# Optimization experiments

Hardware: AMD Instinct MI355X
Metric: run time of the kernel (lower is better)

The kernel has to match this reference:

```python
import jax, jax.numpy as jnp
import numpy as np

TOP_K = 2
NUM_EXPERTS = 64
AUX_COEF = 0.01


def setup_inputs() -> dict:
    key = jax.random.key(0)
    kx, kw = jax.random.split(key)
    B, S, D, E = 4, 4096, 2048, NUM_EXPERTS
    x = jax.random.normal(kx, (B, S, D), dtype=jnp.float32)
    # nn.Linear default init ~ U(-1/sqrt(D), 1/sqrt(D))
    W = jax.random.uniform(kw, (E, D), dtype=jnp.float32,
                           minval=-1.0 / np.sqrt(D), maxval=1.0 / np.sqrt(D))
    return {"x": x, "W": W}


def reference(x, W):
    B, S, D = x.shape
    E = W.shape[0]
    # router projection (no bias)
    logits = jnp.einsum('bsd,ed->bse', x, W)          # [B,S,E]
    probs = jax.nn.softmax(logits, axis=-1)           # [B,S,E]
    top_k_gates, top_k_indices = jax.lax.top_k(probs, TOP_K)  # [B,S,K]
    top_k_gates = top_k_gates / (jnp.sum(top_k_gates, axis=-1, keepdims=True) + 1e-9)
    # aux loss: fraction of routed slots per expert (one-hot mean) x mean router prob
    total_slots = B * S * TOP_K
    counts = jnp.zeros((E,), dtype=jnp.float32).at[top_k_indices.reshape(-1)].add(1.0)
    avg_tokens_per_expert = counts / total_slots      # == one_hot(idx).mean(dims 0,1,2)
    avg_router_prob = jnp.mean(probs, axis=(0, 1))    # [E]
    aux_loss = AUX_COEF * E * jnp.sum(avg_tokens_per_expert * avg_router_prob)
    return top_k_indices, top_k_gates, aux_loss
```

## Files before the change

### kernel.cpp

```cpp
#include <hip/hip_runtime.h>
#include <math.h>

#define NTOK 16384
#define DDIM 2048
#define NEXP 64
#define TMB  64
#define NBLK (NTOK / TMB)
#define CHF  128
#define NCHK (DDIM / CHF)

typedef _Float16 half8v __attribute__((ext_vector_type(8)));
typedef float    f32x4  __attribute__((ext_vector_type(4)));

#define MFMA16(a, b, c) __builtin_amdgcn_mfma_f32_16x16x32_f16((a), (b), (c), 0, 0, 0)

__device__ __forceinline__ void stage16(const void* g, void* l) {
    __builtin_amdgcn_global_load_lds(
        (const __attribute__((address_space(1))) unsigned int*)g,
        (__attribute__((address_space(3))) unsigned int*)l, 16, 0, 0);
}

__device__ __forceinline__ void cvt8(float4 a, float4 b, half8v& h, half8v& l) {
    h[0]=(_Float16)a.x; l[0]=(_Float16)(a.x-(float)h[0]);
    h[1]=(_Float16)a.y; l[1]=(_Float16)(a.y-(float)h[1]);
    h[2]=(_Float16)a.z; l[2]=(_Float16)(a.z-(float)h[2]);
    h[3]=(_Float16)a.w; l[3]=(_Float16)(a.w-(float)h[3]);
    h[4]=(_Float16)b.x; l[4]=(_Float16)(b.x-(float)h[4]);
    h[5]=(_Float16)b.y; l[5]=(_Float16)(b.y-(float)h[5]);
    h[6]=(_Float16)b.z; l[6]=(_Float16)(b.z-(float)h[6]);
    h[7]=(_Float16)b.w; l[7]=(_Float16)(b.w-(float)h[7]);
}

__global__ __launch_bounds__(256, 1) void router_kernel(
    const float* __restrict__ x, const float* __restrict__ W,
    float* __restrict__ accg, float* __restrict__ out)
{
    __shared__ __align__(16) float Xs[2][8192];
    __shared__ __align__(16) float Ws[2][8192];
    __shared__ float lgt[TMB][NEXP + 1];
    __shared__ float cnt[NEXP];
    __shared__ int lastBlk;

    const int tid  = threadIdx.x;
    const int lane = tid & 63;
    const int wv   = __builtin_amdgcn_readfirstlane(tid >> 6);
    const int m0   = blockIdx.x * TMB;

    if (tid < NEXP) cnt[tid] = 0.0f;

#define MKOFF(i) ({ int p_ = (i)*32 + (lane >> 1);                           \
                    int g_ = p_ ^ ((p_ >> 4) & 7);                           \
                    (g_ & 15)*2048 + (g_ >> 6)*32 + ((g_ >> 4) & 3)*8        \
                    + (lane & 1)*4; })
    const int o0 = MKOFF(0), o1 = MKOFF(1), o2 = MKOFF(2), o3 = MKOFF(3);
    const int o4 = MKOFF(4), o5 = MKOFF(5), o6 = MKOFF(6), o7 = MKOFF(7);
#undef MKOFF

    const float* bx = x + (size_t)(m0 + wv * 16) * DDIM;
    const float* bw = W + (size_t)(wv * 16) * DDIM;

#define MKP(S) ({ int g_ = (S)*64 + ((lane >> 4) << 4) + (lane & 15);        \
                  (g_ ^ ((g_ >> 4) & 7)) * 8; })
    const int pf0 = MKP(0), pf1 = MKP(1), pf2 = MKP(2), pf3 = MKP(3);
#undef MKP

    f32x4 acc0 = {0.f,0.f,0.f,0.f}, acc1 = {0.f,0.f,0.f,0.f};
    f32x4 acc2 = {0.f,0.f,0.f,0.f}, acc3 = {0.f,0.f,0.f,0.f};

#define STAGE(cc, B)                                                         \
    {                                                                        \
        const float* bx_ = bx + (size_t)(cc) * CHF;                          \
        const float* bw_ = bw + (size_t)(cc) * CHF;                          \
        float* dx_ = &Xs[B][wv * 2048];                                      \
        float* dw_ = &Ws[B][wv * 2048];                                      \
        stage16(bx_ + o0, dx_ +    0);  stage16(bw_ + o0, dw_ +    0);       \
        stage16(bx_ + o1, dx_ +  256);  stage16(bw_ + o1, dw_ +  256);       \
        stage16(bx_ + o2, dx_ +  512);  stage16(bw_ + o2, dw_ +  512);       \
        stage16(bx_ + o3, dx_ +  768);  stage16(bw_ + o3, dw_ +  768);       \
        stage16(bx_ + o4, dx_ + 1024);  stage16(bw_ + o4, dw_ + 1024);       \
        stage16(bx_ + o5, dx_ + 1280);  stage16(bw_ + o5, dw_ + 1280);       \
        stage16(bx_ + o6, dx_ + 1536);  stage16(bw_ + o6, dw_ + 1536);       \
        stage16(bx_ + o7, dx_ + 1792);  stage16(bw_ + o7, dw_ + 1792);       \
    }

#define STEP(PB, PF)                                                         \
    {                                                                        \
        float4 v0, v1;                                                       \
        half8v bh, bl;                                                       \
        v0 = *(const float4*)&Ws[PB][wv * 2048 + (PF)];                      \
        v1 = *(const float4*)&Ws[PB][wv * 2048 + (PF) + 4];                  \
        cvt8(v0, v1, bh, bl);                                                \
        half8v a0h,a0l,a1h,a1l,a2h,a2l,a3h,a3l;                              \
        v0 = *(const float4*)&Xs[PB][       (PF)];                           \
        v1 = *(const float4*)&Xs[PB][       (PF) + 4];  cvt8(v0,v1,a0h,a0l); \
        v0 = *(const float4*)&Xs[PB][2048 + (PF)];                           \
        v1 = *(const float4*)&Xs[PB][2048 + (PF) + 4];  cvt8(v0,v1,a1h,a1l); \
        v0 = *(const float4*)&Xs[PB][4096 + (PF)];                           \
        v1 = *(const float4*)&Xs[PB][4096 + (PF) + 4];  cvt8(v0,v1,a2h,a2l); \
        v0 = *(const float4*)&Xs[PB][6144 + (PF)];                           \
        v1 = *(const float4*)&Xs[PB][6144 + (PF) + 4];  cvt8(v0,v1,a3h,a3l); \
        acc0 = MFMA16(a0l, bh, acc0);                                        \
        acc0 = MFMA16(a0h, bl, acc0);                                        \
        acc0 = MFMA16(a0h, bh, acc0);                                        \
        acc1 = MFMA16(a1l, bh, acc1);                                        \
        acc1 = MFMA16(a1h, bl, acc1);                                        \
        acc1 = MFMA16(a1h, bh, acc1);                                        \
        acc2 = MFMA16(a2l, bh, acc2);                                        \
        acc2 = MFMA16(a2h, bl, acc2);                                        \
        acc2 = MFMA16(a2h, bh, acc2);                                        \
        acc3 = MFMA16(a3l, bh, acc3);                                        \
        acc3 = MFMA16(a3h, bl, acc3);                                        \
        acc3 = MFMA16(a3h, bh, acc3);                                        \
    }

#define COMPUTE(PB)                                                          \
    STEP(PB, pf0) STEP(PB, pf1) STEP(PB, pf2) STEP(PB, pf3)

    STAGE(0, 0);

    for (int cb = 0; cb < NCHK; cb += 2) {
        __syncthreads();
        STAGE(cb + 1, 1);
        COMPUTE(0);
        __syncthreads();
        if (cb + 2 < NCHK) STAGE(cb + 2, 0);
        COMPUTE(1);
    }
#undef COMPUTE
#undef STEP
#undef STAGE

    {
        const int qr = lane >> 4;
        const int nl = lane & 15;
        #pragma unroll
        for (int rr = 0; rr < 4; ++rr) {
            const int mm = qr * 4 + rr;
            lgt[ 0 + mm][wv * 16 + nl] = acc0[rr];
            lgt[16 + mm][wv * 16 + nl] = acc1[rr];
            lgt[32 + mm][wv * 16 + nl] = acc2[rr];
            lgt[48 + mm][wv * 16 + nl] = acc3[rr];
        }
    }
    __syncthreads();

    for (int pass = 0; pass < 2; ++pass) {
        const int m = pass * 32 + (tid >> 3);
        const int j = tid & 7;
        float l[8];
        #pragma unroll
        for (int i = 0; i < 8; ++i) l[i] = lgt[m][j * 8 + i];

        float mx = l[0];
        #pragma unroll
        for (int i = 1; i < 8; ++i) mx = fmaxf(mx, l[i]);
        #pragma unroll
        for (int off = 1; off < 8; off <<= 1) mx = fmaxf(mx, __shfl_xor(mx, off, 8));

        float ev[8];
        float zs = 0.f;
        float v1 = -INFINITY, v2 = -INFINITY;
        int i1 = 0, i2 = 0;
        #pragma unroll
        for (int i = 0; i < 8; ++i) {
            ev[i] = __expf(l[i] - mx);
            zs += ev[i];
            int e = j * 8 + i;
            if (l[i] > v1)      { v2 = v1; i2 = i1; v1 = l[i]; i1 = e; }
            else if (l[i] > v2) { v2 = l[i]; i2 = e; }
        }
        #pragma unroll
        for (int off = 1; off < 8; off <<= 1) zs += __shfl_xor(zs, off, 8);

        #pragma unroll
        for (int off = 1; off < 8; off <<= 1) {
            float ov1 = __shfl_xor(v1, off, 8);
            int   oi1 = __shfl_xor(i1, off, 8);
            float ov2 = __shfl_xor(v2, off, 8);
            int   oi2 = __shfl_xor(i2, off, 8);
            bool afirst = (v1 > ov1) || (v1 == ov1 && i1 < oi1);
            if (afirst) {
                bool t = (v2 > ov1) || (v2 == ov1 && i2 < oi1);
                v2 = t ? v2 : ov1;
                i2 = t ? i2 : oi1;
            } else {
                bool t = (ov2 > v1) || (ov2 == v1 && oi2 < i1);
                v2 = t ? ov2 : v1;
                i2 = t ? oi2 : i1;
                v1 = ov1;
                i1 = oi1;
            }
        }

        const float invz = 1.0f / zs;
        if (j == 0) {
            float p1 = invz;
            float p2 = __expf(v2 - mx) * invz;
            float sden = p1 + p2 + 1e-9f;
            int tokg = m0 + m;
            out[tokg * 2 + 0] = (float)i1;
            out[tokg * 2 + 1] = (float)i2;
            out[32768 + tokg * 2 + 0] = p1 / sden;
            out[32768 + tokg * 2 + 1] = p2 / sden;
            atomicAdd(&cnt[i1], 1.0f);
            atomicAdd(&cnt[i2], 1.0f);
        }

        #pragma unroll
        for (int i = 0; i < 8; ++i) lgt[m][j * 8 + i] = ev[i] * invz;
    }
    __syncthreads();

    if (tid < NEXP) {
        atomicAdd(&accg[tid], cnt[tid]);
    } else if (tid < 128) {
        int e = tid - 64;
        float s = 0.f;
        #pragma unroll
        for (int t = 0; t < TMB; ++t) s += lgt[t][e];
        atomicAdd(&accg[64 + e], s);
    }
    __syncthreads();

    if (tid == 0) {
        __threadfence();
        unsigned int old = atomicAdd((unsigned int*)(accg + 128), 1u);
        lastBlk = (old == NBLK - 1) ? 1 : 0;
    }
    __syncthreads();
    if (lastBlk && tid < 64) {
        __threadfence();
        const volatile float* ag = accg;
        float c = ag[tid];
        float p = ag[64 + tid];
        float term = (c / (float)(NTOK * 2)) * (p / (float)NTOK);
        #pragma unroll
        for (int off = 1; off < 64; off <<= 1) term += __shfl_xor(term, off, 64);
        if (tid == 0) out[65536] = 0.01f * (float)NEXP * term;
    }
}

extern "C" void kernel_launch(void* const* d_in, const int* in_sizes, int n_in,
                              void* d_out, int out_size, void* d_ws, size_t ws_size,
                              hipStream_t stream) {
    const float* x = (const float*)d_in[0];
    const float* W = (const float*)d_in[1];
    float* out  = (float*)d_out;
    float* accg = (float*)d_ws;

    hipMemsetAsync(accg, 0, 1024, stream);
    router_kernel<<<NBLK, 256, 0, stream>>>(x, W, accg, out);
}
```

Baseline: 220.7 us.

## Split K dimension across block pairs with global partial-logit reduction

Each 64-token tile is now handled by two blocks, each covering half of the hidden dimension. The grid doubles to 512 blocks, and LDS per block halves so two blocks can share a CU. Partial logits go to a global workspace, and the second block of each pair to finish (found via an atomic ticket) sums both halves and runs the softmax/top-k epilogue. The aim is better occupancy and CU fill on a grid that was too small, at the cost of extra global traffic, fences and a serialized epilogue on one block per pair.

```diff
diff --git a/kernel.cpp b/kernel.cpp
--- a/kernel.cpp
+++ b/kernel.cpp
@@ -5,9 +5,10 @@
 #define DDIM 2048
 #define NEXP 64
 #define TMB  64
-#define NBLK (NTOK / TMB)
-#define CHF  128
-#define NCHK (DDIM / CHF)
+#define NBLK 512
+#define KH   1024
+#define CHF  64
+#define NCHK (KH / CHF)
 
 typedef _Float16 half8v __attribute__((ext_vector_type(8)));
 typedef float    f32x4  __attribute__((ext_vector_type(4)));
@@ -31,37 +32,38 @@
     h[7]=(_Float16)b.w; l[7]=(_Float16)(b.w-(float)h[7]);
 }
 
-__global__ __launch_bounds__(256, 1) void router_kernel(
+__global__ __launch_bounds__(256, 2) void router_kernel(
     const float* __restrict__ x, const float* __restrict__ W,
-    float* __restrict__ accg, float* __restrict__ out)
+    float* __restrict__ accg, unsigned int* __restrict__ gtick,
+    unsigned int* __restrict__ ptick, float* __restrict__ P,
+    float* __restrict__ out)
 {
-    __shared__ __align__(16) float Xs[2][8192];
-    __shared__ __align__(16) float Ws[2][8192];
-    __shared__ float lgt[TMB][NEXP + 1];
-    __shared__ float cnt[NEXP];
-    __shared__ int lastBlk;
+    __shared__ __align__(16) float smem[16384];
+    __shared__ int winFlag, lastFlag;
+
+    float (*Xs)[4096] = (float(*)[4096])smem;
+    float (*Ws)[4096] = (float(*)[4096])(smem + 8192);
 
     const int tid  = threadIdx.x;
     const int lane = tid & 63;
     const int wv   = __builtin_amdgcn_readfirstlane(tid >> 6);
-    const int m0   = blockIdx.x * TMB;
-
-    if (tid < NEXP) cnt[tid] = 0.0f;
+    const int pair = blockIdx.x >> 1;
+    const int kh   = blockIdx.x & 1;
+    const int m0   = pair * TMB;
 
 #define MKOFF(i) ({ int p_ = (i)*32 + (lane >> 1);                           \
                     int g_ = p_ ^ ((p_ >> 4) & 7);                           \
-                    (g_ & 15)*2048 + (g_ >> 6)*32 + ((g_ >> 4) & 3)*8        \
+                    (g_ & 15)*DDIM + ((g_ >> 6) & 1)*32 + ((g_ >> 4) & 3)*8  \
                     + (lane & 1)*4; })
     const int o0 = MKOFF(0), o1 = MKOFF(1), o2 = MKOFF(2), o3 = MKOFF(3);
-    const int o4 = MKOFF(4), o5 = MKOFF(5), o6 = MKOFF(6), o7 = MKOFF(7);
 #undef MKOFF
 
-    const float* bx = x + (size_t)(m0 + wv * 16) * DDIM;
-    const float* bw = W + (size_t)(wv * 16) * DDIM;
+    const float* bx = x + (size_t)(m0 + wv * 16) * DDIM + kh * KH;
+    const float* bw = W + (size_t)(wv * 16) * DDIM + kh * KH;
 
 #define MKP(S) ({ int g_ = (S)*64 + ((lane >> 4) << 4) + (lane & 15);        \
                   (g_ ^ ((g_ >> 4) & 7)) * 8; })
-    const int pf0 = MKP(0), pf1 = MKP(1), pf2 = MKP(2), pf3 = MKP(3);
+    const int pf0 = MKP(0), pf1 = MKP(1);
 #undef MKP
 
     f32x4 acc0 = {0.f,0.f,0.f,0.f}, acc1 = {0.f,0.f,0.f,0.f};
@@ -71,34 +73,30 @@
     {                                                                        \
         const float* bx_ = bx + (size_t)(cc) * CHF;                          \
         const float* bw_ = bw + (size_t)(cc) * CHF;                          \
-        float* dx_ = &Xs[B][wv * 2048];                                      \
-        float* dw_ = &Ws[B][wv * 2048];                                      \
-        stage16(bx_ + o0, dx_ +    0);  stage16(bw_ + o0, dw_ +    0);       \
-        stage16(bx_ + o1, dx_ +  256);  stage16(bw_ + o1, dw_ +  256);       \
-        stage16(bx_ + o2, dx_ +  512);  stage16(bw_ + o2, dw_ +  512);       \
-        stage16(bx_ + o3, dx_ +  768);  stage16(bw_ + o3, dw_ +  768);       \
-        stage16(bx_ + o4, dx_ + 1024);  stage16(bw_ + o4, dw_ + 1024);       \
-        stage16(bx_ + o5, dx_ + 1280);  stage16(bw_ + o5, dw_ + 1280);       \
-        stage16(bx_ + o6, dx_ + 1536);  stage16(bw_ + o6, dw_ + 1536);       \
-        stage16(bx_ + o7, dx_ + 1792);  stage16(bw_ + o7, dw_ + 1792);       \
+        float* dx_ = &Xs[B][wv * 1024];                                      \
+        float* dw_ = &Ws[B][wv * 1024];                                      \
+        stage16(bx_ + o0, dx_ +   0);  stage16(bw_ + o0, dw_ +   0);         \
+        stage16(bx_ + o1, dx_ + 256);  stage16(bw_ + o1, dw_ + 256);         \
+        stage16(bx_ + o2, dx_ + 512);  stage16(bw_ + o2, dw_ + 512);         \
+        stage16(bx_ + o3, dx_ + 768);  stage16(bw_ + o3, dw_ + 768);         \
     }
 
 #define STEP(PB, PF)                                                         \
     {                                                                        \
         float4 v0, v1;                                                       \
         half8v bh, bl;                                                       \
-        v0 = *(const float4*)&Ws[PB][wv * 2048 + (PF)];                      \
-        v1 = *(const float4*)&Ws[PB][wv * 2048 + (PF) + 4];                  \
+        v0 = *(const float4*)&Ws[PB][wv * 1024 + (PF)];                      \
+        v1 = *(const float4*)&Ws[PB][wv * 1024 + (PF) + 4];                  \
         cvt8(v0, v1, bh, bl);                                                \
         half8v a0h,a0l,a1h,a1l,a2h,a2l,a3h,a3l;                              \
         v0 = *(const float4*)&Xs[PB][       (PF)];                           \
         v1 = *(const float4*)&Xs[PB][       (PF) + 4];  cvt8(v0,v1,a0h,a0l); \
+        v0 = *(const float4*)&Xs[PB][1024 + (PF)];                           \
+        v1 = *(const float4*)&Xs[PB][1024 + (PF) + 4];  cvt8(v0,v1,a1h,a1l); \
         v0 = *(const float4*)&Xs[PB][2048 + (PF)];                           \
-        v1 = *(const float4*)&Xs[PB][2048 + (PF) + 4];  cvt8(v0,v1,a1h,a1l); \
-        v0 = *(const float4*)&Xs[PB][4096 + (PF)];                           \
-        v1 = *(const float4*)&Xs[PB][4096 + (PF) + 4];  cvt8(v0,v1,a2h,a2l); \
-        v0 = *(const float4*)&Xs[PB][6144 + (PF)];                           \
-        v1 = *(const float4*)&Xs[PB][6144 + (PF) + 4];  cvt8(v0,v1,a3h,a3l); \
+        v1 = *(const float4*)&Xs[PB][2048 + (PF) + 4];  cvt8(v0,v1,a2h,a2l); \
+        v0 = *(const float4*)&Xs[PB][3072 + (PF)];                           \
+        v1 = *(const float4*)&Xs[PB][3072 + (PF) + 4];  cvt8(v0,v1,a3h,a3l); \
         acc0 = MFMA16(a0l, bh, acc0);                                        \
         acc0 = MFMA16(a0h, bl, acc0);                                        \
         acc0 = MFMA16(a0h, bh, acc0);                                        \
@@ -113,36 +111,58 @@
         acc3 = MFMA16(a3h, bh, acc3);                                        \
     }
 
-#define COMPUTE(PB)                                                          \
-    STEP(PB, pf0) STEP(PB, pf1) STEP(PB, pf2) STEP(PB, pf3)
-
     STAGE(0, 0);
-
     for (int cb = 0; cb < NCHK; cb += 2) {
         __syncthreads();
         STAGE(cb + 1, 1);
-        COMPUTE(0);
+        STEP(0, pf0) STEP(0, pf1)
         __syncthreads();
         if (cb + 2 < NCHK) STAGE(cb + 2, 0);
-        COMPUTE(1);
-    }
-#undef COMPUTE
+        STEP(1, pf0) STEP(1, pf1)
+    }
 #undef STEP
 #undef STAGE
 
     {
         const int qr = lane >> 4;
         const int nl = lane & 15;
+        float* gp = P + (size_t)blockIdx.x * 4096 + (qr * 4) * NEXP + wv * 16 + nl;
         #pragma unroll
         for (int rr = 0; rr < 4; ++rr) {
-            const int mm = qr * 4 + rr;
-            lgt[ 0 + mm][wv * 16 + nl] = acc0[rr];
-            lgt[16 + mm][wv * 16 + nl] = acc1[rr];
-            lgt[32 + mm][wv * 16 + nl] = acc2[rr];
-            lgt[48 + mm][wv * 16 + nl] = acc3[rr];
-        }
-    }
-    __syncthreads();
+            gp[(     rr) * NEXP] = acc0[rr];
+            gp[(16 + rr) * NEXP] = acc1[rr];
+            gp[(32 + rr) * NEXP] = acc2[rr];
+            gp[(48 + rr) * NEXP] = acc3[rr];
+        }
+    }
+    __threadfence();
+    __syncthreads();
+    if (tid == 0) {
+        unsigned int old = atomicAdd(&ptick[pair], 1u);
+        winFlag = (old == 1u);
+    }
+    __syncthreads();
+    if (!winFlag) return;
+
+    __threadfence();
+    {
+        float (*lgt)[NEXP + 1] = (float(*)[NEXP + 1])smem;
+        const volatile float* p0 = P + (size_t)(pair * 2 + 0) * 4096;
+        const volatile float* p1 = P + (size_t)(pair * 2 + 1) * 4096;
+        #pragma unroll
+        for (int i = 0; i < 16; ++i) {
+            int idx = tid * 16 + i;
+            lgt[idx >> 6][idx & 63] = p0[idx] + p1[idx];
+        }
+    }
+    {
+        float* cnt = smem + 8192;
+        if (tid < NEXP) cnt[tid] = 0.0f;
+    }
+    __syncthreads();
+
+    float (*lgt)[NEXP + 1] = (float(*)[NEXP + 1])smem;
+    float* cnt = smem + 8192;
 
     for (int pass = 0; pass < 2; ++pass) {
         const int m = pass * 32 + (tid >> 3);
@@ -194,14 +214,14 @@
 
         const float invz = 1.0f / zs;
         if (j == 0) {
-            float p1 = invz;
-            float p2 = __expf(v2 - mx) * invz;
-            float sden = p1 + p2 + 1e-9f;
+            float p1v = invz;
+            float p2v = __expf(v2 - mx) * invz;
+            float sden = p1v + p2v + 1e-9f;
             int tokg = m0 + m;
             out[tokg * 2 + 0] = (float)i1;
             out[tokg * 2 + 1] = (float)i2;
-            out[32768 + tokg * 2 + 0] = p1 / sden;
-            out[32768 + tokg * 2 + 1] = p2 / sden;
+            out[32768 + tokg * 2 + 0] = p1v / sden;
+            out[32768 + tokg * 2 + 1] = p2v / sden;
             atomicAdd(&cnt[i1], 1.0f);
             atomicAdd(&cnt[i2], 1.0f);
         }
@@ -224,11 +244,11 @@
 
     if (tid == 0) {
         __threadfence();
-        unsigned int old = atomicAdd((unsigned int*)(accg + 128), 1u);
-        lastBlk = (old == NBLK - 1) ? 1 : 0;
-    }
-    __syncthreads();
-    if (lastBlk && tid < 64) {
+        unsigned int old = atomicAdd(gtick, 1u);
+        lastFlag = (old == (NBLK / 2 - 1)) ? 1 : 0;
+    }
+    __syncthreads();
+    if (lastFlag && tid < 64) {
         __threadfence();
         const volatile float* ag = accg;
         float c = ag[tid];
@@ -247,7 +267,10 @@
     const float* W = (const float*)d_in[1];
     float* out  = (float*)d_out;
     float* accg = (float*)d_ws;
-
-    hipMemsetAsync(accg, 0, 1024, stream);
-    router_kernel<<<NBLK, 256, 0, stream>>>(x, W, accg, out);
-}
+    unsigned int* gtick = (unsigned int*)(accg + 128);
+    unsigned int* ptick = (unsigned int*)(accg + 132);
+    float* P = (float*)((char*)d_ws + 4096);
+
+    hipMemsetAsync(d_ws, 0, 2048, stream);
+    router_kernel<<<NBLK, 256, 0, stream>>>(x, W, accg, gtick, ptick, P, out);
+}
```

Measured after the change: 315.8 us. 43.1% more time.
